# Performance work log

Hardware: AMD Instinct MI355X
Metric: run time of the kernel (lower is better)

Reference implementation:

```python
import jax, jax.numpy as jnp
import numpy as np

N_PIX = 12 * 128**2   # 196608, full-sky HEALPix n_side=128
MAX_NEIGHBORS = 32
BATCH = 8
CHANNELS = 4


def setup_inputs() -> dict:
    key = jax.random.key(0)
    k1, k2, k3 = jax.random.split(key, 3)
    x = jax.random.normal(k1, (BATCH, N_PIX, CHANNELS), dtype=jnp.float32)
    # Gaussian kernel values exp(-0.5 r^2 / sigma^2) are in (0, 1]; uniform positives mimic this.
    kernel_k = jax.random.uniform(k2, (N_PIX, MAX_NEIGHBORS), dtype=jnp.float32)
    inds_k = jax.random.randint(k3, (N_PIX, MAX_NEIGHBORS), 0, N_PIX, dtype=jnp.int64)
    return {"x": x, "kernel_k": kernel_k, "inds_k": inds_k}


def reference(x, kernel_k, inds_k):
    # Faithful to HealpixSmoothingLayer:
    #   sparse kernel K[p, inds_k[p,k]] = kernel_k[p,k]
    #   normalization: K_norm[i,j] = K[i,j] / rowsum(j)  (col_sum over axis=1, broadcast over axis=0)
    #   output[b,p,c] = sum_j K_norm[p,j] * x[b,j,c]  (sparse_dense_matmul per channel)
    rowsum = jnp.sum(kernel_k, axis=1)                 # [N]
    w = kernel_k / rowsum[inds_k]                      # [N, K] normalized weights
    xg = x[:, inds_k, :]                               # [B, N, K, C] neighbor gather
    return jnp.einsum("nk,bnkc->bnc", w, xg)          # [B, N, C]
```

## Files before the change

### kernel.cpp

```cpp
#include <hip/hip_runtime.h>
#include <hip/hip_bf16.h>
#include <hip/hip_fp16.h>

#define N_PIX 196608
#define KNN 32
#define BATCH 8

typedef float f4v __attribute__((ext_vector_type(4)));

#define XS_BYTES ((size_t)N_PIX * 32 * 2)

__device__ __forceinline__ unsigned int pack_h2(float a, float b) {
    __half2 h = __floats2half2_rn(a, b);
    return *reinterpret_cast<unsigned int*>(&h);
}

__global__ __launch_bounds__(256) void k_prep(const float* __restrict__ x,
                                              const float* __restrict__ kern,
                                              const unsigned int* __restrict__ inds_u32,
                                              uint2* __restrict__ xs,
                                              int* __restrict__ flag) {
    if (blockIdx.x == 0 && threadIdx.x < 64) {
        unsigned int v = inds_u32[threadIdx.x * 2 + 1];
        unsigned long long bal = __ballot(v != 0);
        if (threadIdx.x == 0) *flag = (bal == 0ULL) ? 1 : 0;
    }

    __shared__ float s_inv[32];
    __shared__ uint2 tile[32][9];
    int n0 = blockIdx.x * 32;
    int t = threadIdx.x;

    const float4* kv = reinterpret_cast<const float4*>(kern);
    float4 v = kv[(size_t)(n0 + (t >> 3)) * 8 + (t & 7)];
    float s = v.x + v.y + v.z + v.w;
    s += __shfl_xor(s, 1);
    s += __shfl_xor(s, 2);
    s += __shfl_xor(s, 4);
    if ((t & 7) == 0) s_inv[t >> 3] = 1.0f / s;
    __syncthreads();

    int b = t >> 5, i = t & 31;
    const float4* xv = reinterpret_cast<const float4*>(x);
    float4 u = xv[(size_t)b * N_PIX + n0 + i];
    float r = s_inv[i];
    uint2 p;
    p.x = pack_h2(u.x * r, u.y * r);
    p.y = pack_h2(u.z * r, u.w * r);
    tile[i][b] = p;
    __syncthreads();

    int row = t >> 3, bb = t & 7;
    xs[(size_t)(n0 + row) * 8 + bb] = tile[row][bb];
}

template <int STRIDE>
__device__ __forceinline__ void main_body(int n, int b, const float* __restrict__ kern,
                                          const char* __restrict__ ipb,
                                          const uint2* __restrict__ xsv,
                                          float* __restrict__ out) {
    const f4v* wv = reinterpret_cast<const f4v*>(kern) + (size_t)n * 8;
    f4v acc = (f4v)0.0f;

#pragma unroll 2
    for (int k0 = 0; k0 < KNN; k0 += 4) {
        int j[4];
#pragma unroll
        for (int u = 0; u < 4; ++u)
            j[u] = __builtin_nontemporal_load(
                reinterpret_cast<const int*>(ipb + (size_t)(k0 + u) * STRIDE));
        f4v wq = __builtin_nontemporal_load(wv + (k0 >> 2));

        uint2 g[4];
#pragma unroll
        for (int u = 0; u < 4; ++u) g[u] = xsv[(size_t)j[u] * 8 + b];
#pragma unroll
        for (int u = 0; u < 4; ++u) {
            float2 f0 = __half22float2(*reinterpret_cast<__half2*>(&g[u].x));
            float2 f1 = __half22float2(*reinterpret_cast<__half2*>(&g[u].y));
            float w = wq[u];
            acc[0] = fmaf(w, f0.x, acc[0]);
            acc[1] = fmaf(w, f0.y, acc[1]);
            acc[2] = fmaf(w, f1.x, acc[2]);
            acc[3] = fmaf(w, f1.y, acc[3]);
        }
    }
    __builtin_nontemporal_store(acc,
        reinterpret_cast<f4v*>(out) + ((size_t)b * N_PIX + n));
}

__global__ __launch_bounds__(256, 8) void k_main(const float* __restrict__ kern,
                                                 const void* __restrict__ inds,
                                                 const uint2* __restrict__ xs,
                                                 const int* __restrict__ flag,
                                                 float* __restrict__ out) {
    int tid = blockIdx.x * 256 + threadIdx.x;
    int n = tid >> 3;
    int b = tid & 7;
    const char* base = reinterpret_cast<const char*>(inds);
    if (*flag) {
        main_body<8>(n, b, kern, base + (size_t)n * KNN * 8, xs, out);
    } else {
        main_body<4>(n, b, kern, base + (size_t)n * KNN * 4, xs, out);
    }
}

extern "C" void kernel_launch(void* const* d_in, const int* in_sizes, int n_in,
                              void* d_out, int out_size, void* d_ws, size_t ws_size,
                              hipStream_t stream) {
    const float* x    = (const float*)d_in[0];
    const float* kern = (const float*)d_in[1];
    const void*  inds = d_in[2];
    float* out = (float*)d_out;

    uint2* xs  = (uint2*)d_ws;
    int*  flag = (int*)((char*)d_ws + XS_BYTES);

    k_prep<<<N_PIX / 32, 256, 0, stream>>>(x, kern, (const unsigned int*)inds, xs, flag);
    k_main<<<(N_PIX * BATCH) / 256, 256, 0, stream>>>(kern, inds, xs, flag, out);
}
```

Baseline: 210.7 us.

## Pack indices with quantized weights and split gather into two batch halves

Adds a pre-pass that packs each neighbor index (18 bits) and its kernel weight quantized to 14 bits into one 32-bit word. The x table is re-laid out as two batch-half planes, so the main kernel can run twice, each time over half the batches with a smaller gather working set. The aim is to cut index and weight bandwidth in the main loop and to improve cache locality of the random gathers. In exchange it adds extra launches and extra passes over the inputs, and the 14-bit weight quantization costs accuracy.

```diff
diff --git a/kernel.cpp b/kernel.cpp
--- a/kernel.cpp
+++ b/kernel.cpp
@@ -1,108 +1,112 @@
 #include <hip/hip_runtime.h>
-#include <hip/hip_bf16.h>
 #include <hip/hip_fp16.h>
 
 #define N_PIX 196608
 #define KNN 32
-#define BATCH 8
 
 typedef float f4v __attribute__((ext_vector_type(4)));
+typedef unsigned int u4v __attribute__((ext_vector_type(4)));
 
-#define XS_BYTES ((size_t)N_PIX * 32 * 2)
+#define XS_BYTES ((size_t)N_PIX * 64)
+#define PK_BYTES ((size_t)N_PIX * KNN * 4)
+#define RS_BYTES ((size_t)N_PIX * 4)
 
 __device__ __forceinline__ unsigned int pack_h2(float a, float b) {
     __half2 h = __floats2half2_rn(a, b);
     return *reinterpret_cast<unsigned int*>(&h);
 }
 
-__global__ __launch_bounds__(256) void k_prep(const float* __restrict__ x,
-                                              const float* __restrict__ kern,
-                                              const unsigned int* __restrict__ inds_u32,
-                                              uint2* __restrict__ xs,
-                                              int* __restrict__ flag) {
-    if (blockIdx.x == 0 && threadIdx.x < 64) {
-        unsigned int v = inds_u32[threadIdx.x * 2 + 1];
-        unsigned long long bal = __ballot(v != 0);
-        if (threadIdx.x == 0) *flag = (bal == 0ULL) ? 1 : 0;
+__global__ void k_detect(const unsigned int* __restrict__ inds_u32, int* __restrict__ flag) {
+    unsigned int v = inds_u32[threadIdx.x * 2 + 1];
+    unsigned long long bal = __ballot(v != 0);
+    if (threadIdx.x == 0) *flag = (bal == 0ULL) ? 1 : 0;
+}
+
+template <int STRIDE>
+__device__ __forceinline__ void pack_body(int n, int k4, const char* __restrict__ ib,
+                                          const float* __restrict__ kern,
+                                          unsigned int* __restrict__ packed,
+                                          float* __restrict__ inv_rs) {
+    int j[4];
+    if (STRIDE == 8) {
+        const u4v* p = reinterpret_cast<const u4v*>(ib + (size_t)n * KNN * 8 + k4 * 32);
+        u4v a = p[0], b = p[1];
+        j[0] = a.x; j[1] = a.z; j[2] = b.x; j[3] = b.z;
+    } else {
+        u4v a = *reinterpret_cast<const u4v*>(ib + (size_t)n * KNN * 4 + k4 * 16);
+        j[0] = a.x; j[1] = a.y; j[2] = a.z; j[3] = a.w;
     }
-
-    __shared__ float s_inv[32];
-    __shared__ uint2 tile[32][9];
-    int n0 = blockIdx.x * 32;
-    int t = threadIdx.x;
-
-    const float4* kv = reinterpret_cast<const float4*>(kern);
-    float4 v = kv[(size_t)(n0 + (t >> 3)) * 8 + (t & 7)];
-    float s = v.x + v.y + v.z + v.w;
+    f4v kv = *reinterpret_cast<const f4v*>(kern + (size_t)n * KNN + k4 * 4);
+    float s = kv[0] + kv[1] + kv[2] + kv[3];
     s += __shfl_xor(s, 1);
     s += __shfl_xor(s, 2);
     s += __shfl_xor(s, 4);
-    if ((t & 7) == 0) s_inv[t >> 3] = 1.0f / s;
-    __syncthreads();
+    if (k4 == 0) inv_rs[n] = 1.0f / s;
+    u4v pk;
+#pragma unroll
+    for (int u = 0; u < 4; ++u) {
+        unsigned int wq = (unsigned int)__float2int_rn(kv[u] * 16383.0f);
+        wq = wq > 16383u ? 16383u : wq;
+        pk[u] = ((unsigned int)j[u] << 14) | wq;
+    }
+    *reinterpret_cast<u4v*>(packed + (size_t)n * KNN + k4 * 4) = pk;
+}
 
+__global__ __launch_bounds__(256) void k_pack(const float* __restrict__ kern,
+                                              const void* __restrict__ inds,
+                                              const int* __restrict__ flag,
+                                              unsigned int* __restrict__ packed,
+                                              float* __restrict__ inv_rs) {
+    int tid = blockIdx.x * 256 + threadIdx.x;
+    int n = tid >> 3, k4 = tid & 7;
+    const char* ib = reinterpret_cast<const char*>(inds);
+    if (*flag) pack_body<8>(n, k4, ib, kern, packed, inv_rs);
+    else       pack_body<4>(n, k4, ib, kern, packed, inv_rs);
+}
+
+__global__ __launch_bounds__(256) void k_xs(const float* __restrict__ x,
+                                            const float* __restrict__ inv_rs,
+                                            uint2* __restrict__ xs) {
+    __shared__ uint2 tile[32][9];
+    int n0 = blockIdx.x * 32, t = threadIdx.x;
     int b = t >> 5, i = t & 31;
-    const float4* xv = reinterpret_cast<const float4*>(x);
-    float4 u = xv[(size_t)b * N_PIX + n0 + i];
-    float r = s_inv[i];
+    f4v u = reinterpret_cast<const f4v*>(x)[(size_t)b * N_PIX + n0 + i];
+    float r = inv_rs[n0 + i];
     uint2 p;
-    p.x = pack_h2(u.x * r, u.y * r);
-    p.y = pack_h2(u.z * r, u.w * r);
+    p.x = pack_h2(u[0] * r, u[1] * r);
+    p.y = pack_h2(u[2] * r, u[3] * r);
     tile[i][b] = p;
     __syncthreads();
-
-    int row = t >> 3, bb = t & 7;
-    xs[(size_t)(n0 + row) * 8 + bb] = tile[row][bb];
+    int P = t >> 7, rem = t & 127, row = rem >> 2, bq = rem & 3;
+    xs[((size_t)P * N_PIX + n0 + row) * 4 + bq] = tile[row][P * 4 + bq];
 }
 
-template <int STRIDE>
-__device__ __forceinline__ void main_body(int n, int b, const float* __restrict__ kern,
-                                          const char* __restrict__ ipb,
-                                          const uint2* __restrict__ xsv,
-                                          float* __restrict__ out) {
-    const f4v* wv = reinterpret_cast<const f4v*>(kern) + (size_t)n * 8;
+__global__ __launch_bounds__(256, 8) void k_gmain(const unsigned int* __restrict__ packed,
+                                                  const uint2* __restrict__ xsh,
+                                                  float* __restrict__ outh) {
+    int tid = blockIdx.x * 256 + threadIdx.x;
+    int n = tid >> 2, bq = tid & 3;
+    const u4v* pk = reinterpret_cast<const u4v*>(packed) + (size_t)n * 8;
     f4v acc = (f4v)0.0f;
 
 #pragma unroll 2
-    for (int k0 = 0; k0 < KNN; k0 += 4) {
-        int j[4];
-#pragma unroll
-        for (int u = 0; u < 4; ++u)
-            j[u] = __builtin_nontemporal_load(
-                reinterpret_cast<const int*>(ipb + (size_t)(k0 + u) * STRIDE));
-        f4v wq = __builtin_nontemporal_load(wv + (k0 >> 2));
-
+    for (int k0 = 0; k0 < 8; ++k0) {
+        u4v pq = __builtin_nontemporal_load(pk + k0);
         uint2 g[4];
 #pragma unroll
-        for (int u = 0; u < 4; ++u) g[u] = xsv[(size_t)j[u] * 8 + b];
+        for (int u = 0; u < 4; ++u) g[u] = xsh[(size_t)(pq[u] >> 14) * 4 + bq];
 #pragma unroll
         for (int u = 0; u < 4; ++u) {
+            float w = (float)(pq[u] & 0x3FFFu) * (1.0f / 16383.0f);
             float2 f0 = __half22float2(*reinterpret_cast<__half2*>(&g[u].x));
             float2 f1 = __half22float2(*reinterpret_cast<__half2*>(&g[u].y));
-            float w = wq[u];
             acc[0] = fmaf(w, f0.x, acc[0]);
             acc[1] = fmaf(w, f0.y, acc[1]);
             acc[2] = fmaf(w, f1.x, acc[2]);
             acc[3] = fmaf(w, f1.y, acc[3]);
         }
     }
-    __builtin_nontemporal_store(acc,
-        reinterpret_cast<f4v*>(out) + ((size_t)b * N_PIX + n));
-}
-
-__global__ __launch_bounds__(256, 8) void k_main(const float* __restrict__ kern,
-                                                 const void* __restrict__ inds,
-                                                 const uint2* __restrict__ xs,
-                                                 const int* __restrict__ flag,
-                                                 float* __restrict__ out) {
-    int tid = blockIdx.x * 256 + threadIdx.x;
-    int n = tid >> 3;
-    int b = tid & 7;
-    const char* base = reinterpret_cast<const char*>(inds);
-    if (*flag) {
-        main_body<8>(n, b, kern, base + (size_t)n * KNN * 8, xs, out);
-    } else {
-        main_body<4>(n, b, kern, base + (size_t)n * KNN * 4, xs, out);
-    }
+    __builtin_nontemporal_store(acc, reinterpret_cast<f4v*>(outh) + (size_t)bq * N_PIX + n);
 }
 
 extern "C" void kernel_launch(void* const* d_in, const int* in_sizes, int n_in,
@@ -113,9 +117,15 @@
     const void*  inds = d_in[2];
     float* out = (float*)d_out;
 
-    uint2* xs  = (uint2*)d_ws;
-    int*  flag = (int*)((char*)d_ws + XS_BYTES);
+    uint2*        xs     = (uint2*)d_ws;
+    unsigned int* packed = (unsigned int*)((char*)d_ws + XS_BYTES);
+    float*        inv_rs = (float*)((char*)d_ws + XS_BYTES + PK_BYTES);
+    int*          flag   = (int*)((char*)d_ws + XS_BYTES + PK_BYTES + RS_BYTES);
 
-    k_prep<<<N_PIX / 32, 256, 0, stream>>>(x, kern, (const unsigned int*)inds, xs, flag);
-    k_main<<<(N_PIX * BATCH) / 256, 256, 0, stream>>>(kern, inds, xs, flag, out);
+    k_detect<<<1, 64, 0, stream>>>((const unsigned int*)inds, flag);
+    k_pack<<<(N_PIX * 8) / 256, 256, 0, stream>>>(kern, inds, flag, packed, inv_rs);
+    k_xs<<<N_PIX / 32, 256, 0, stream>>>(x, inv_rs, xs);
+    k_gmain<<<(N_PIX * 4) / 256, 256, 0, stream>>>(packed, xs, out);
+    k_gmain<<<(N_PIX * 4) / 256, 256, 0, stream>>>(packed, xs + (size_t)N_PIX * 4,
+                                                   out + (size_t)N_PIX * 16);
 }
```

New measurement: 231.3 us. +9.8%, slower.
